# Kernel optimization log

Hardware: AMD Instinct MI355X
Metric: run time of the kernel (lower is better)

## Reference

```python
import jax, jax.numpy as jnp
import numpy as np

B, TGT, SRC, SRC_DIM, TGT_DIM = 4, 4096, 4096, 256, 256
NEG_BIG = 1.0e11   # additive mask constant from the torch code
CLAMP_MIN = -1.0e10


def setup_inputs() -> dict:
    key = jax.random.key(0)
    k1, k2, k3, k4 = jax.random.split(key, 4)
    h_t = jax.random.normal(k1, (B, TGT, TGT_DIM), dtype=jnp.float32)
    h_s = jax.random.normal(k2, (B, SRC, SRC_DIM), dtype=jnp.float32)
    m_s = jax.random.randint(k3, (B, SRC), 0, 2, dtype=jnp.int32)
    # linear_in: nn.Linear(src_dim, tgt_dim, bias=False) -> weight [tgt_dim, src_dim]
    lim = float(np.sqrt(1.0 / SRC_DIM))
    W_in = jax.random.uniform(k4, (TGT_DIM, SRC_DIM), dtype=jnp.float32, minval=-lim, maxval=lim)
    return {"h_t": h_t, "h_s": h_s, "m_s": m_s, "W_in": W_in}


def reference(h_t, h_s, m_s, W_in):
    # 'general' score: h_t @ (linear_in(h_s))^T
    energy = jnp.einsum("bsd,td->bst", h_s, W_in)          # (B, S, tgt_dim)
    scores = jnp.einsum("btd,bsd->bts", h_t, energy)        # (B, T, S)
    m = m_s.astype(scores.dtype)[:, None, :]                 # (B, 1, S)
    scores = scores * m - NEG_BIG * (1.0 - m)
    scores = jax.nn.softmax(jnp.maximum(scores, CLAMP_MIN), axis=-1)
    context = jnp.einsum("bts,bsd->btd", scores, h_s)        # (B, T, src_dim)
    return context, scores
```

## Files before the change

### kernel.cpp

```cpp
#include <hip/hip_runtime.h>
#include <cstdint>
#include <cstddef>

typedef _Float16 f16;
typedef _Float16 half8 __attribute__((ext_vector_type(8)));
typedef float floatx4 __attribute__((ext_vector_type(4)));
typedef unsigned short ushort8 __attribute__((ext_vector_type(8)));

__device__ __forceinline__ void gload_lds16(const void* g, void* l) {
    __builtin_amdgcn_global_load_lds(
        (const __attribute__((address_space(1))) void*)g,
        (__attribute__((address_space(3))) void*)l,
        16, 0, 0);
}

__device__ __forceinline__ unsigned short f32_to_bf16(float f) {
    unsigned u = __float_as_uint(f);
    return (unsigned short)((u + 0x7FFFu + ((u >> 16) & 1u)) >> 16);
}
__device__ __forceinline__ float bf16_to_f32(unsigned short h) {
    return __uint_as_float(((unsigned)h) << 16);
}

__global__ void k_cvt2(const float* __restrict__ srcA, f16* __restrict__ dstA, int n8a,
                       const float* __restrict__ srcB, f16* __restrict__ dstB, int n8b) {
    int i = blockIdx.x * blockDim.x + threadIdx.x;
    const float* src;
    f16* dst;
    int j;
    if (i < n8a) { src = srcA; dst = dstA; j = i; }
    else { j = i - n8a; if (j >= n8b) return; src = srcB; dst = dstB; }
    const float4* s = (const float4*)src + 2 * (size_t)j;
    float4 a = s[0], b = s[1];
    half8 h;
    h[0] = (f16)a.x; h[1] = (f16)a.y; h[2] = (f16)a.z; h[3] = (f16)a.w;
    h[4] = (f16)b.x; h[5] = (f16)b.y; h[6] = (f16)b.z; h[7] = (f16)b.w;
    ((half8*)dst)[j] = h;
}

__global__ void k_hs(const float* __restrict__ hs, f16* __restrict__ hs16, f16* __restrict__ hsT) {
    int id = blockIdx.x;
    int dt = id & 3;
    int st = (id >> 2) & 63;
    int b  = id >> 8;
    __shared__ f16 tile[64][65];
    int t = threadIdx.x;
    int s0 = st * 64, d0 = dt * 64;
#pragma unroll
    for (int i = 0; i < 16; i++) {
        int e = t + i * 256;
        int r = e >> 6, c = e & 63;
        float v = hs[((size_t)(b * 4096 + s0 + r)) * 256 + d0 + c];
        f16 hv = (f16)v;
        hs16[((size_t)(b * 4096 + s0 + r)) * 256 + d0 + c] = hv;
        tile[r][c] = hv;
    }
    __syncthreads();
#pragma unroll
    for (int i = 0; i < 16; i++) {
        int e = t + i * 256;
        int r = e >> 6, c = e & 63;
        hsT[((size_t)(b * 256 + d0 + r)) * 4096 + s0 + c] = tile[c][r];
    }
}

__global__ __launch_bounds__(256, 2) void k_energy(
    const f16* __restrict__ A,
    const f16* __restrict__ Bt,
    f16* __restrict__ C)
{
    int id = blockIdx.x;
    int tn = id & 1, tm = (id >> 1) & 31, b = id >> 6;
    const f16* Ab = A + (size_t)b * 4096 * 256;

    __shared__ __align__(16) f16 As[128 * 64];
    __shared__ __align__(16) f16 Bs[128 * 64];

    int tid = threadIdx.x;
    int wave = tid >> 6, lane = tid & 63;
    int wr = wave >> 1, wc = wave & 1;
    int lm = lane & 15, lq = lane >> 4;

    floatx4 acc[4][4] = {};
    int r0 = tm * 128, c0 = tn * 128;

    for (int k0 = 0; k0 < 256; k0 += 64) {
#pragma unroll
        for (int i = 0; i < 4; i++) {
            int rbase = wave * 32 + i * 8;
            int row = rbase + (lane >> 3);
            gload_lds16(Ab + (size_t)(r0 + row) * 256 + k0 + (lane & 7) * 8, &As[rbase * 64]);
            gload_lds16(Bt + (size_t)(c0 + row) * 256 + k0 + (lane & 7) * 8, &Bs[rbase * 64]);
        }
        __syncthreads();
        half8 af[4][2], bf[4][2];
#pragma unroll
        for (int mi = 0; mi < 4; mi++)
#pragma unroll
            for (int kk = 0; kk < 2; kk++) {
                af[mi][kk] = *(const half8*)&As[(wr * 64 + mi * 16 + lm) * 64 + kk * 32 + lq * 8];
                bf[mi][kk] = *(const half8*)&Bs[(wc * 64 + mi * 16 + lm) * 64 + kk * 32 + lq * 8];
            }
#pragma unroll
        for (int kk = 0; kk < 2; kk++)
#pragma unroll
            for (int mi = 0; mi < 4; mi++)
#pragma unroll
                for (int ni = 0; ni < 4; ni++)
                    acc[mi][ni] = __builtin_amdgcn_mfma_f32_16x16x32_f16(af[mi][kk], bf[ni][kk], acc[mi][ni], 0, 0, 0);
        __syncthreads();
    }
#pragma unroll
    for (int mi = 0; mi < 4; mi++)
#pragma unroll
        for (int ni = 0; ni < 4; ni++)
#pragma unroll
            for (int r = 0; r < 4; r++) {
                int row = r0 + wr * 64 + mi * 16 + lq * 4 + r;
                int col = c0 + wc * 64 + ni * 16 + lm;
                C[(size_t)(b * 4096 + row) * 256 + col] = (f16)acc[mi][ni][r];
            }
}

__global__ __launch_bounds__(256, 2) void k_scores(
    const f16* __restrict__ A,
    const f16* __restrict__ Bt,
    const int* __restrict__ ms,
    unsigned short* __restrict__ E,
    float* __restrict__ rsum)
{
    int id = blockIdx.x;
    int tn = id & 31, tm = (id >> 5) & 31, b = id >> 10;
    const f16* Ab = A + (size_t)b * 4096 * 256;
    const f16* Bb = Bt + (size_t)b * 4096 * 256;

    __shared__ __align__(16) f16 As[128 * 64];
    __shared__ __align__(16) f16 Bs[128 * 64];

    int tid = threadIdx.x;
    int wave = tid >> 6, lane = tid & 63;
    int wr = wave >> 1, wc = wave & 1;
    int lm = lane & 15, lq = lane >> 4;

    floatx4 acc[4][4] = {};
    int r0 = tm * 128, c0 = tn * 128;

    for (int k0 = 0; k0 < 256; k0 += 64) {
#pragma unroll
        for (int i = 0; i < 4; i++) {
            int rbase = wave * 32 + i * 8;
            int row = rbase + (lane >> 3);
            gload_lds16(Ab + (size_t)(r0 + row) * 256 + k0 + (lane & 7) * 8, &As[rbase * 64]);
            gload_lds16(Bb + (size_t)(c0 + row) * 256 + k0 + (lane & 7) * 8, &Bs[rbase * 64]);
        }
        __syncthreads();
        half8 af[4][2], bf[4][2];
#pragma unroll
        for (int mi = 0; mi < 4; mi++)
#pragma unroll
            for (int kk = 0; kk < 2; kk++) {
                af[mi][kk] = *(const half8*)&As[(wr * 64 + mi * 16 + lm) * 64 + kk * 32 + lq * 8];
                bf[mi][kk] = *(const half8*)&Bs[(wc * 64 + mi * 16 + lm) * 64 + kk * 32 + lq * 8];
            }
#pragma unroll
        for (int kk = 0; kk < 2; kk++)
#pragma unroll
            for (int mi = 0; mi < 4; mi++)
#pragma unroll
                for (int ni = 0; ni < 4; ni++)
                    acc[mi][ni] = __builtin_amdgcn_mfma_f32_16x16x32_f16(af[mi][kk], bf[ni][kk], acc[mi][ni], 0, 0, 0);
        __syncthreads();
    }
    float rs[4][4] = {};
#pragma unroll
    for (int ni = 0; ni < 4; ni++) {
        int col = c0 + wc * 64 + ni * 16 + lm;
        int m = ms[b * 4096 + col];
#pragma unroll
        for (int mi = 0; mi < 4; mi++)
#pragma unroll
            for (int r = 0; r < 4; r++) {
                int row = r0 + wr * 64 + mi * 16 + lq * 4 + r;
                float e = m ? __expf(acc[mi][ni][r]) : 0.0f;
                E[(size_t)(b * 4096 + row) * 4096 + col] = f32_to_bf16(e);
                rs[mi][r] += e;
            }
    }
#pragma unroll
    for (int mi = 0; mi < 4; mi++)
#pragma unroll
        for (int r = 0; r < 4; r++) {
            float v = rs[mi][r];
#pragma unroll
            for (int off = 1; off < 16; off <<= 1)
                v += __shfl_xor(v, off, 16);
            if (lm == 0) {
                int row = r0 + wr * 64 + mi * 16 + lq * 4 + r;
                atomicAdd(&rsum[b * 4096 + row], v);
            }
        }
}

__global__ __launch_bounds__(256, 2) void k_ctx(
    const f16* __restrict__ BtT,
    const unsigned short* __restrict__ E,
    float* __restrict__ P,
    const float* __restrict__ rsum,
    f16* __restrict__ part)
{
    int id = blockIdx.x;
    int ks = id & 3, tt = (id >> 2) & 31, b = id >> 7;
    int tid = threadIdx.x;
    int wave = tid >> 6, lane = tid & 63;
    int lm = lane & 15, lq = lane >> 4;

    __shared__ __align__(16) f16 Bs0[8 * 2048];
    __shared__ __align__(16) f16 Bs1[8 * 2048];

    int t0 = tt * 128;
    const f16* Bb = BtT + (size_t)b * 256 * 4096;

    float rinv[2];
    size_t rowbase[2];
#pragma unroll
    for (int mi = 0; mi < 2; mi++) {
        int row = t0 + wave * 32 + mi * 16 + lm;
        int gr = b * 4096 + row;
        rinv[mi] = 1.0f / rsum[gr];
        rowbase[mi] = (size_t)gr * 4096;
    }

    int g0 = wave * 2, g1 = wave * 2 + 1;
    int c0g = 2 * (g0 & 3), c1g = 2 * (g1 & 3);
    const f16* gp0 = Bb + (size_t)(lane ^ c0g) * 4096 + g0 * 8;
    const f16* gp1 = Bb + (size_t)(lane ^ c1g) * 4096 + g1 * 8;
    int lds_off0 = g0 * 2048, lds_off1 = g1 * 2048;

    int rbk[2];
    rbk[0] = (0 * 4 + lq) * 2048 + (lm ^ (2 * lq)) * 8;
    rbk[1] = (1 * 4 + lq) * 2048 + (lm ^ (2 * lq)) * 8;

    floatx4 acc[2][16] = {};
    int sbeg = ks * 1024;

#pragma unroll
    for (int R = 0; R < 256; R += 64) {
        gload_lds16(gp0 + (size_t)R * 4096 + sbeg, &Bs0[lds_off0 + R * 8]);
        gload_lds16(gp1 + (size_t)R * 4096 + sbeg, &Bs0[lds_off1 + R * 8]);
    }
    __syncthreads();

#define CTX_ITER(IT, BSR, BSW) do { \
    int s0c_ = sbeg + (IT) * 64; \
    ushort8 ev_[2][2]; \
    _Pragma("unroll") \
    for (int mi = 0; mi < 2; mi++) \
        _Pragma("unroll") \
        for (int kk = 0; kk < 2; kk++) \
            ev_[mi][kk] = *(const ushort8*)(E + rowbase[mi] + s0c_ + kk * 32 + lq * 8); \
    if ((IT) < 15) { \
        int s0n_ = s0c_ + 64; \
        _Pragma("unroll") \
        for (int R = 0; R < 256; R += 64) { \
            gload_lds16(gp0 + (size_t)R * 4096 + s0n_, &BSW[lds_off0 + R * 8]); \
            gload_lds16(gp1 + (size_t)R * 4096 + s0n_, &BSW[lds_off1 + R * 8]); \
        } \
    } \
    half8 af_[2][2]; \
    _Pragma("unroll") \
    for (int mi = 0; mi < 2; mi++) \
        _Pragma("unroll") \
        for (int kk = 0; kk < 2; kk++) { \
            half8 h_; \
            _Pragma("unroll") \
            for (int j = 0; j < 8; j++) \
                h_[j] = (f16)(bf16_to_f32(ev_[mi][kk][j]) * rinv[mi]); \
            af_[mi][kk] = h_; \
        } \
    _Pragma("unroll") \
    for (int mi = 0; mi < 2; mi++) \
        _Pragma("unroll") \
        for (int kk = 0; kk < 2; kk++) { \
            float* p_ = P + rowbase[mi] + s0c_ + kk * 32 + lq * 8; \
            half8 h_ = af_[mi][kk]; \
            ((float4*)p_)[0] = make_float4((float)h_[0], (float)h_[1], (float)h_[2], (float)h_[3]); \
            ((float4*)p_)[1] = make_float4((float)h_[4], (float)h_[5], (float)h_[6], (float)h_[7]); \
        } \
    _Pragma("unroll") \
    for (int kk = 0; kk < 2; kk++) \
        _Pragma("unroll") \
        for (int ni = 0; ni < 16; ni++) { \
            half8 bf_ = *(const half8*)&BSR[rbk[kk] + ni * 128]; \
            _Pragma("unroll") \
            for (int mi = 0; mi < 2; mi++) \
                acc[mi][ni] = __builtin_amdgcn_mfma_f32_16x16x32_f16(af_[mi][kk], bf_, acc[mi][ni], 0, 0, 0); \
        } \
    __syncthreads(); \
    } while (0)

    for (int it = 0; it < 16; it += 2) {
        CTX_ITER(it, Bs0, Bs1);
        CTX_ITER(it + 1, Bs1, Bs0);
    }
#undef CTX_ITER

    f16* Pp = part + (size_t)ks * 4194304 + (size_t)b * 1048576;
#pragma unroll
    for (int mi = 0; mi < 2; mi++)
#pragma unroll
        for (int ni = 0; ni < 16; ni++)
#pragma unroll
            for (int r = 0; r < 4; r++) {
                int row = t0 + wave * 32 + mi * 16 + lq * 4 + r;
                int col = ni * 16 + lm;
                Pp[(size_t)row * 256 + col] = (f16)acc[mi][ni][r];
            }
}

__global__ void k_red(const f16* __restrict__ part, float* __restrict__ out) {
    size_t i = (size_t)blockIdx.x * 256 + threadIdx.x;
    const half8* p = (const half8*)part;
    half8 a = p[i];
    half8 b = p[i + 524288];
    half8 c = p[i + 1048576];
    half8 d = p[i + 1572864];
    float4 o0, o1;
    o0.x = (float)a[0] + (float)b[0] + (float)c[0] + (float)d[0];
    o0.y = (float)a[1] + (float)b[1] + (float)c[1] + (float)d[1];
    o0.z = (float)a[2] + (float)b[2] + (float)c[2] + (float)d[2];
    o0.w = (float)a[3] + (float)b[3] + (float)c[3] + (float)d[3];
    o1.x = (float)a[4] + (float)b[4] + (float)c[4] + (float)d[4];
    o1.y = (float)a[5] + (float)b[5] + (float)c[5] + (float)d[5];
    o1.z = (float)a[6] + (float)b[6] + (float)c[6] + (float)d[6];
    o1.w = (float)a[7] + (float)b[7] + (float)c[7] + (float)d[7];
    ((float4*)out)[2 * i] = o0;
    ((float4*)out)[2 * i + 1] = o1;
}

extern "C" void kernel_launch(void* const* d_in, const int* in_sizes, int n_in,
                              void* d_out, int out_size, void* d_ws, size_t ws_size,
                              hipStream_t stream) {
    const float* h_t = (const float*)d_in[0];
    const float* h_s = (const float*)d_in[1];
    const int*   m_s = (const int*)d_in[2];
    const float* W   = (const float*)d_in[3];

    float* out = (float*)d_out;
    char* ws = (char*)d_ws;
    f16* h_t16 = (f16*)(ws);
    f16* h_s16 = (f16*)(ws + 8388608);
    f16* h_sT  = (f16*)(ws + 16777216);
    f16* en16  = (f16*)(ws + 25165824);
    f16* W16   = (f16*)(ws + 33554432);
    float* rsum = (float*)(ws + 33685504);
    unsigned short* e16 = (unsigned short*)(ws + 33751040);
    f16* part = (f16*)(ws + 167968768);

    float* ctx = out;
    float* sc  = out + 4194304;

    hipMemsetAsync(rsum, 0, 16384 * sizeof(float), stream);
    k_cvt2<<<2080, 256, 0, stream>>>(h_t, h_t16, 524288, W, W16, 8192);
    k_hs<<<1024, 256, 0, stream>>>(h_s, h_s16, h_sT);
    k_energy<<<256, 256, 0, stream>>>(h_s16, W16, en16);
    k_scores<<<4096, 256, 0, stream>>>(h_t16, en16, m_s, e16, rsum);
    k_ctx<<<512, 256, 0, stream>>>(h_sT, e16, sc, rsum, part);
    k_red<<<2048, 256, 0, stream>>>(part, ctx);
}
```

Baseline: 490.7 us.

## Drop split-K in context kernel, use smaller row tiles with XCD-aware mapping

The context GEMM no longer splits the source dimension into four partial sums written as fp16 and then reduced by a separate kernel. Each block now covers a 32-row tile over the full 4096-long source dimension, with four waves in a 2x2 arrangement, and writes fp32 output directly. The block index is remapped so each XCD handles one batch, which should improve L2 reuse of the shared h_sT panel. This removes the partial-buffer traffic and one launch, but each block now streams the whole B panel through LDS for only 32 rows, which raises LDS and L2 load per FLOP.

```diff
diff --git a/kernel.cpp b/kernel.cpp
--- a/kernel.cpp
+++ b/kernel.cpp
@@ -206,29 +206,27 @@
     const unsigned short* __restrict__ E,
     float* __restrict__ P,
     const float* __restrict__ rsum,
-    f16* __restrict__ part)
+    float* __restrict__ ctx)
 {
     int id = blockIdx.x;
-    int ks = id & 3, tt = (id >> 2) & 31, b = id >> 7;
+    int xcd = id & 7;
+    int b = xcd >> 1;
+    int tt = (id >> 3) + ((xcd & 1) << 6);
     int tid = threadIdx.x;
     int wave = tid >> 6, lane = tid & 63;
     int lm = lane & 15, lq = lane >> 4;
+    int wr = wave >> 1, wc = wave & 1;
 
     __shared__ __align__(16) f16 Bs0[8 * 2048];
     __shared__ __align__(16) f16 Bs1[8 * 2048];
 
-    int t0 = tt * 128;
+    int t0 = tt * 32;
     const f16* Bb = BtT + (size_t)b * 256 * 4096;
 
-    float rinv[2];
-    size_t rowbase[2];
-#pragma unroll
-    for (int mi = 0; mi < 2; mi++) {
-        int row = t0 + wave * 32 + mi * 16 + lm;
-        int gr = b * 4096 + row;
-        rinv[mi] = 1.0f / rsum[gr];
-        rowbase[mi] = (size_t)gr * 4096;
-    }
+    int row = t0 + wr * 16 + lm;
+    int gr = b * 4096 + row;
+    float rinv = 1.0f / rsum[gr];
+    size_t rowbase = (size_t)gr * 4096;
 
     int g0 = wave * 2, g1 = wave * 2 + 1;
     int c0g = 2 * (g0 & 3), c1g = 2 * (g1 & 3);
@@ -237,28 +235,25 @@
     int lds_off0 = g0 * 2048, lds_off1 = g1 * 2048;
 
     int rbk[2];
-    rbk[0] = (0 * 4 + lq) * 2048 + (lm ^ (2 * lq)) * 8;
-    rbk[1] = (1 * 4 + lq) * 2048 + (lm ^ (2 * lq)) * 8;
-
-    floatx4 acc[2][16] = {};
-    int sbeg = ks * 1024;
+    rbk[0] = (0 * 4 + lq) * 2048 + (lm ^ (2 * lq)) * 8 + wc * 1024;
+    rbk[1] = (1 * 4 + lq) * 2048 + (lm ^ (2 * lq)) * 8 + wc * 1024;
+
+    floatx4 acc[8] = {};
 
 #pragma unroll
     for (int R = 0; R < 256; R += 64) {
-        gload_lds16(gp0 + (size_t)R * 4096 + sbeg, &Bs0[lds_off0 + R * 8]);
-        gload_lds16(gp1 + (size_t)R * 4096 + sbeg, &Bs0[lds_off1 + R * 8]);
+        gload_lds16(gp0 + (size_t)R * 4096, &Bs0[lds_off0 + R * 8]);
+        gload_lds16(gp1 + (size_t)R * 4096, &Bs0[lds_off1 + R * 8]);
     }
     __syncthreads();
 
 #define CTX_ITER(IT, BSR, BSW) do { \
-    int s0c_ = sbeg + (IT) * 64; \
-    ushort8 ev_[2][2]; \
+    int s0c_ = (IT) * 64; \
+    ushort8 ev_[2]; \
     _Pragma("unroll") \
-    for (int mi = 0; mi < 2; mi++) \
-        _Pragma("unroll") \
-        for (int kk = 0; kk < 2; kk++) \
-            ev_[mi][kk] = *(const ushort8*)(E + rowbase[mi] + s0c_ + kk * 32 + lq * 8); \
-    if ((IT) < 15) { \
+    for (int kk = 0; kk < 2; kk++) \
+        ev_[kk] = *(const ushort8*)(E + rowbase + s0c_ + kk * 32 + lq * 8); \
+    if ((IT) < 63) { \
         int s0n_ = s0c_ + 64; \
         _Pragma("unroll") \
         for (int R = 0; R < 256; R += 64) { \
@@ -266,75 +261,46 @@
             gload_lds16(gp1 + (size_t)R * 4096 + s0n_, &BSW[lds_off1 + R * 8]); \
         } \
     } \
-    half8 af_[2][2]; \
+    half8 af_[2]; \
     _Pragma("unroll") \
-    for (int mi = 0; mi < 2; mi++) \
+    for (int kk = 0; kk < 2; kk++) { \
+        half8 h_; \
         _Pragma("unroll") \
-        for (int kk = 0; kk < 2; kk++) { \
-            half8 h_; \
-            _Pragma("unroll") \
-            for (int j = 0; j < 8; j++) \
-                h_[j] = (f16)(bf16_to_f32(ev_[mi][kk][j]) * rinv[mi]); \
-            af_[mi][kk] = h_; \
-        } \
+        for (int j = 0; j < 8; j++) \
+            h_[j] = (f16)(bf16_to_f32(ev_[kk][j]) * rinv); \
+        af_[kk] = h_; \
+    } \
     _Pragma("unroll") \
-    for (int mi = 0; mi < 2; mi++) \
-        _Pragma("unroll") \
-        for (int kk = 0; kk < 2; kk++) { \
-            float* p_ = P + rowbase[mi] + s0c_ + kk * 32 + lq * 8; \
-            half8 h_ = af_[mi][kk]; \
-            ((float4*)p_)[0] = make_float4((float)h_[0], (float)h_[1], (float)h_[2], (float)h_[3]); \
-            ((float4*)p_)[1] = make_float4((float)h_[4], (float)h_[5], (float)h_[6], (float)h_[7]); \
-        } \
+    for (int kk = 0; kk < 2; kk++) { \
+        float* p_ = P + rowbase + s0c_ + kk * 32 + lq * 8; \
+        half8 h_ = af_[kk]; \
+        ((float4*)p_)[0] = make_float4((float)h_[0], (float)h_[1], (float)h_[2], (float)h_[3]); \
+        ((float4*)p_)[1] = make_float4((float)h_[4], (float)h_[5], (float)h_[6], (float)h_[7]); \
+    } \
     _Pragma("unroll") \
     for (int kk = 0; kk < 2; kk++) \
         _Pragma("unroll") \
-        for (int ni = 0; ni < 16; ni++) { \
+        for (int ni = 0; ni < 8; ni++) { \
             half8 bf_ = *(const half8*)&BSR[rbk[kk] + ni * 128]; \
-            _Pragma("unroll") \
-            for (int mi = 0; mi < 2; mi++) \
-                acc[mi][ni] = __builtin_amdgcn_mfma_f32_16x16x32_f16(af_[mi][kk], bf_, acc[mi][ni], 0, 0, 0); \
+            acc[ni] = __builtin_amdgcn_mfma_f32_16x16x32_f16(af_[kk], bf_, acc[ni], 0, 0, 0); \
         } \
     __syncthreads(); \
     } while (0)
 
-    for (int it = 0; it < 16; it += 2) {
+    for (int it = 0; it < 64; it += 2) {
         CTX_ITER(it, Bs0, Bs1);
         CTX_ITER(it + 1, Bs1, Bs0);
     }
 #undef CTX_ITER
 
-    f16* Pp = part + (size_t)ks * 4194304 + (size_t)b * 1048576;
-#pragma unroll
-    for (int mi = 0; mi < 2; mi++)
-#pragma unroll
-        for (int ni = 0; ni < 16; ni++)
-#pragma unroll
-            for (int r = 0; r < 4; r++) {
-                int row = t0 + wave * 32 + mi * 16 + lq * 4 + r;
-                int col = ni * 16 + lm;
-                Pp[(size_t)row * 256 + col] = (f16)acc[mi][ni][r];
-            }
-}
-
-__global__ void k_red(const f16* __restrict__ part, float* __restrict__ out) {
-    size_t i = (size_t)blockIdx.x * 256 + threadIdx.x;
-    const half8* p = (const half8*)part;
-    half8 a = p[i];
-    half8 b = p[i + 524288];
-    half8 c = p[i + 1048576];
-    half8 d = p[i + 1572864];
-    float4 o0, o1;
-    o0.x = (float)a[0] + (float)b[0] + (float)c[0] + (float)d[0];
-    o0.y = (float)a[1] + (float)b[1] + (float)c[1] + (float)d[1];
-    o0.z = (float)a[2] + (float)b[2] + (float)c[2] + (float)d[2];
-    o0.w = (float)a[3] + (float)b[3] + (float)c[3] + (float)d[3];
-    o1.x = (float)a[4] + (float)b[4] + (float)c[4] + (float)d[4];
-    o1.y = (float)a[5] + (float)b[5] + (float)c[5] + (float)d[5];
-    o1.z = (float)a[6] + (float)b[6] + (float)c[6] + (float)d[6];
-    o1.w = (float)a[7] + (float)b[7] + (float)c[7] + (float)d[7];
-    ((float4*)out)[2 * i] = o0;
-    ((float4*)out)[2 * i + 1] = o1;
+#pragma unroll
+    for (int ni = 0; ni < 8; ni++)
+#pragma unroll
+        for (int r = 0; r < 4; r++) {
+            int orow = t0 + wr * 16 + lq * 4 + r;
+            int col = wc * 128 + ni * 16 + lm;
+            ctx[(size_t)(b * 4096 + orow) * 256 + col] = acc[ni][r];
+        }
 }
 
 extern "C" void kernel_launch(void* const* d_in, const int* in_sizes, int n_in,
@@ -354,7 +320,6 @@
     f16* W16   = (f16*)(ws + 33554432);
     float* rsum = (float*)(ws + 33685504);
     unsigned short* e16 = (unsigned short*)(ws + 33751040);
-    f16* part = (f16*)(ws + 167968768);
 
     float* ctx = out;
     float* sc  = out + 4194304;
@@ -364,6 +329,5 @@
     k_hs<<<1024, 256, 0, stream>>>(h_s, h_s16, h_sT);
     k_energy<<<256, 256, 0, stream>>>(h_s16, W16, en16);
     k_scores<<<4096, 256, 0, stream>>>(h_t16, en16, m_s, e16, rsum);
-    k_ctx<<<512, 256, 0, stream>>>(h_sT, e16, sc, rsum, part);
-    k_red<<<2048, 256, 0, stream>>>(part, ctx);
-}
+    k_ctx<<<512, 256, 0, stream>>>(h_sT, e16, sc, rsum, ctx);
+}
```

Result: slower. 607.6 us (+23.8%).
